# Performance work log

Hardware: AMD Instinct MI355X
Metric: run time of the kernel (lower is better)

The kernel has to match this reference:

```python
import jax, jax.numpy as jnp
import numpy as np

NUM_HEADS = 12
HEAD_DIM = 64
DIM = NUM_HEADS * HEAD_DIM  # 768
WIN = 14
REL = 2 * WIN - 1  # 27


def setup_inputs() -> dict:
    key = jax.random.key(0)
    ks = jax.random.split(key, 7)
    B, N = 256, WIN * WIN
    return {
        "x": jax.random.normal(ks[0], (B, N, DIM), dtype=jnp.float32),
        "qkv_w": jax.random.normal(ks[1], (3 * DIM, DIM), dtype=jnp.float32) * 0.02,
        "qkv_b": jnp.zeros((3 * DIM,), dtype=jnp.float32),
        "rel_pos_h": jax.random.normal(ks[2], (REL, HEAD_DIM), dtype=jnp.float32) * 0.02,
        "rel_pos_w": jax.random.normal(ks[3], (REL, HEAD_DIM), dtype=jnp.float32) * 0.02,
        "proj_w": jax.random.normal(ks[4], (DIM, DIM), dtype=jnp.float32) * 0.02,
        "proj_b": jnp.zeros((DIM,), dtype=jnp.float32),
        "H": WIN,
        "W": WIN,
    }


def _rel_pos_bias(q, rel_pos_h, rel_pos_w, H, W):
    # q: [B, heads, H*W, d] (already scaled). q_shape == k_shape == (H, W), ratios == 1.
    dist_h = jnp.arange(H)[:, None] - jnp.arange(H)[None, :] + (H - 1)  # [H, H]
    dist_w = jnp.arange(W)[:, None] - jnp.arange(W)[None, :] + (W - 1)  # [W, W]
    Rh = rel_pos_h[dist_h]  # [H, H, d]
    Rw = rel_pos_w[dist_w]  # [W, W, d]
    B, nh = q.shape[0], q.shape[1]
    r_q = q.reshape(B, nh, H, W, q.shape[-1])
    rel_h = jnp.einsum("bnhwd,hkd->bnhwk", r_q, Rh)  # [B, nh, H, W, Hk]
    rel_w = jnp.einsum("bnhwd,wkd->bnhwk", r_q, Rw)  # [B, nh, H, W, Wk]
    return rel_h[..., :, None] + rel_w[..., None, :]  # [B, nh, H, W, Hk, Wk]


def reference(x, qkv_w, qkv_b, rel_pos_h, rel_pos_w, proj_w, proj_b, H, W):
    B, N, C = x.shape
    d = C // NUM_HEADS
    scale = d ** -0.5
    qkv = x @ qkv_w.T + qkv_b  # [B, N, 3C]
    qkv = qkv.reshape(B, N, 3, NUM_HEADS, d).transpose(2, 0, 3, 1, 4)
    q, k, v = qkv[0], qkv[1], qkv[2]  # [B, nh, N, d]
    q = q * scale
    attn = jnp.einsum("bhqd,bhkd->bhqk", q, k)  # [B, nh, N, N]
    bias = _rel_pos_bias(q, rel_pos_h, rel_pos_w, H, W)
    attn = (attn.reshape(B, NUM_HEADS, H, W, H, W) + bias).reshape(B, NUM_HEADS, N, N)
    attn = jax.nn.softmax(attn, axis=-1)
    out = jnp.einsum("bhqk,bhkd->bhqd", attn, v)  # [B, nh, N, d]
    out = out.transpose(0, 2, 1, 3).reshape(B, N, C)
    return out @ proj_w.T + proj_b
```

## Files before the change

kernel.cpp:

```cpp
#include <hip/hip_runtime.h>
#include <stdint.h>


typedef __attribute__((ext_vector_type(8))) short bf16x8;
typedef __attribute__((ext_vector_type(4))) float f32x4;
typedef unsigned short u16;
typedef unsigned int u32;

__device__ __forceinline__ u16 f2bf(float f) {
  u32 x = __float_as_uint(f);
  x += 0x7fffu + ((x >> 16) & 1u);
  return (u16)(x >> 16);
}

__device__ __forceinline__ void gload_lds16(const void* g, void* l) {
  __builtin_amdgcn_global_load_lds(
      (__attribute__((address_space(1))) void*)g,
      (__attribute__((address_space(3))) void*)l, 16, 0, 0);
}

__global__ __launch_bounds__(256) void cvt_bf16(const float* __restrict__ src,
                                                u16* __restrict__ dst, int n4) {
  int i = blockIdx.x * 256 + threadIdx.x;
  if (i < n4) {
    float4 f = ((const float4*)src)[i];
    uint2 p;
    p.x = (u32)f2bf(f.x) | ((u32)f2bf(f.y) << 16);
    p.y = (u32)f2bf(f.z) | ((u32)f2bf(f.w) << 16);
    ((uint2*)dst)[i] = p;
  }
}

template <int MODE>
__global__ __launch_bounds__(256) void gemm128(
    const u16* __restrict__ A, const u16* __restrict__ W,
    const float* __restrict__ bias, u16* __restrict__ qb, u16* __restrict__ kb,
    u16* __restrict__ vb, float* __restrict__ outf) {
  __shared__ u16 As[128 * 32];
  __shared__ u16 Bs[128 * 32];
  const int t = threadIdx.x;
  const int m0 = blockIdx.y << 7;
  const int n0 = blockIdx.x << 7;
  const int lane = t & 63, wv = t >> 6;
  const int quad = lane >> 4, l15 = lane & 15;
  const int wm = (wv >> 1) << 6, wn = (wv & 1) << 6;

  f32x4 acc[4][4];
#pragma unroll
  for (int i = 0; i < 4; i++)
#pragma unroll
    for (int j = 0; j < 4; j++) acc[i][j] = (f32x4){0.f, 0.f, 0.f, 0.f};

  const int c0 = t, c1 = t + 256;
  const u16* gA0 = A + (size_t)(m0 + (c0 >> 2)) * 768 + (c0 & 3) * 8;
  const u16* gA1 = A + (size_t)(m0 + (c1 >> 2)) * 768 + (c1 & 3) * 8;
  const u16* gB0 = W + (size_t)(n0 + (c0 >> 2)) * 768 + (c0 & 3) * 8;
  const u16* gB1 = W + (size_t)(n0 + (c1 >> 2)) * 768 + (c1 & 3) * 8;
  u16* lA0 = As + c0 * 8;  u16* lA1 = As + c1 * 8;
  u16* lB0 = Bs + c0 * 8;  u16* lB1 = Bs + c1 * 8;

  const u16* pA = As + (wm + l15) * 32 + quad * 8;
  const u16* pB = Bs + (wn + l15) * 32 + quad * 8;

  for (int k0 = 0; k0 < 768; k0 += 32) {
    __syncthreads();
    gload_lds16(gA0 + k0, lA0);
    gload_lds16(gA1 + k0, lA1);
    gload_lds16(gB0 + k0, lB0);
    gload_lds16(gB1 + k0, lB1);
    __syncthreads();
    bf16x8 af[4], bfr[4];
#pragma unroll
    for (int i = 0; i < 4; i++) af[i] = *(const bf16x8*)(pA + i * 16 * 32);
#pragma unroll
    for (int j = 0; j < 4; j++) bfr[j] = *(const bf16x8*)(pB + j * 16 * 32);
#pragma unroll
    for (int i = 0; i < 4; i++)
#pragma unroll
      for (int j = 0; j < 4; j++)
        acc[i][j] =
            __builtin_amdgcn_mfma_f32_16x16x32_bf16(af[i], bfr[j], acc[i][j], 0, 0, 0);
  }

  if (MODE == 0) {
#pragma unroll
    for (int j = 0; j < 4; j++) {
      int n = n0 + wn + j * 16 + l15;
      int which = n / 768;
      int cc = n - which * 768;
      int head = cc >> 6, dch = cc & 63;
      float bs = bias[n];
      u16* dst = (which == 0) ? qb : ((which == 1) ? kb : vb);
      float sc = (which == 0) ? 0.125f : 1.0f;
#pragma unroll
      for (int i = 0; i < 4; i++) {
#pragma unroll
        for (int r = 0; r < 4; r++) {
          int m = m0 + wm + i * 16 + (quad << 2) + r;
          int bb = m / 196, tok = m - bb * 196;
          float v = (acc[i][j][r] + bs) * sc;
          dst[((size_t)(bb * 12 + head) * 196 + tok) * 64 + dch] = f2bf(v);
        }
      }
    }
  } else {
#pragma unroll
    for (int j = 0; j < 4; j++) {
      int n = n0 + wn + j * 16 + l15;
      float bs = bias[n];
#pragma unroll
      for (int i = 0; i < 4; i++) {
#pragma unroll
        for (int r = 0; r < 4; r++) {
          int m = m0 + wm + i * 16 + (quad << 2) + r;
          outf[(size_t)m * 768 + n] = acc[i][j][r] + bs;
        }
      }
    }
  }
}

__global__ __launch_bounds__(256) void attn_fused(
    const u16* __restrict__ qbuf, const u16* __restrict__ kbuf,
    const u16* __restrict__ vbuf, const float* __restrict__ rel_h,
    const float* __restrict__ rel_w, u16* __restrict__ aout) {
  __shared__ u16 Vt[26 * 512];
  __shared__ u16 PsArr[4 * 26 * 128];

  const int t = threadIdx.x;
  const int bh = blockIdx.x;
  const int b = bh / 12, h = bh - b * 12;
  const int lane = t & 63, wv = t >> 6;
  const int quad = lane >> 4, l15 = lane & 15;
  const size_t base = (size_t)bh * (196 * 64);

  u16* Ps = PsArr + wv * (26 * 128);
  float* Tf = (float*)Ps;

  for (int c = t; c < 196 * 8; c += 256) {
    int row = c >> 3, seg = c & 7;
    uint4 vv = *(const uint4*)(vbuf + base + row * 64 + seg * 8);
    const u16* pv8 = (const u16*)&vv;
    u16* dst = Vt + (row >> 3) * 512 + (row & 7);
#pragma unroll
    for (int e = 0; e < 8; e++) dst[(seg * 8 + e) * 8] = pv8[e];
  }
  for (int i = t; i < 12 * 64; i += 256) {
    int k = 196 + (i >> 6), d = i & 63;
    Vt[(k >> 3) * 512 + d * 8 + (k & 7)] = 0;
  }

  bf16x8 brl[2][2][2];
#pragma unroll
  for (int half = 0; half < 2; half++) {
    const float* relp = half ? rel_w : rel_h;
#pragma unroll
    for (int nt = 0; nt < 2; nt++) {
      int ridx = nt * 16 + l15;
      if (ridx > 26) ridx = 26;
#pragma unroll
      for (int ks = 0; ks < 2; ks++) {
        const float* p = relp + ridx * 64 + ks * 32 + quad * 8;
        float4 f0 = *(const float4*)p;
        float4 f1 = *(const float4*)(p + 4);
        bf16x8 r;
        r[0] = (short)f2bf(f0.x); r[1] = (short)f2bf(f0.y);
        r[2] = (short)f2bf(f0.z); r[3] = (short)f2bf(f0.w);
        r[4] = (short)f2bf(f1.x); r[5] = (short)f2bf(f1.y);
        r[6] = (short)f2bf(f1.z); r[7] = (short)f2bf(f1.w);
        brl[half][nt][ks] = r;
      }
    }
  }
  __syncthreads();

  for (int qt = wv; qt < 13; qt += 4) {
    int qrl = qt * 16 + l15;
    if (qrl > 195) qrl = 195;
    bf16x8 aq0 = *(const bf16x8*)(qbuf + base + qrl * 64 + quad * 8);
    bf16x8 aq1 = *(const bf16x8*)(qbuf + base + qrl * 64 + 32 + quad * 8);

#pragma unroll
    for (int half = 0; half < 2; half++) {
#pragma unroll
      for (int nt = 0; nt < 2; nt++) {
        f32x4 tc = (f32x4){0.f, 0.f, 0.f, 0.f};
        tc = __builtin_amdgcn_mfma_f32_16x16x32_bf16(aq0, brl[half][nt][0], tc, 0, 0, 0);
        tc = __builtin_amdgcn_mfma_f32_16x16x32_bf16(aq1, brl[half][nt][1], tc, 0, 0, 0);
        int col = nt * 16 + l15;
        if (col < 27) {
#pragma unroll
          for (int r = 0; r < 4; r++)
            Tf[half * 448 + (quad * 4 + r) * 28 + col] = tc[r];
        }
      }
    }

    int trow[4], hqv[4], wqv[4];
#pragma unroll
    for (int r = 0; r < 4; r++) {
      int qr = qt * 16 + quad * 4 + r;
      if (qr > 195) qr = 195;
      hqv[r] = qr / 14;
      wqv[r] = qr - hqv[r] * 14;
      trow[r] = (quad * 4 + r) * 28;
    }

    u32 pw2[13][2];
    float sm[4] = {0.f, 0.f, 0.f, 0.f};
#pragma unroll
    for (int kt = 0; kt < 13; kt++) {
      int key = kt * 16 + l15;
      int keyc = (key > 195) ? 195 : key;
      bool valid = (key < 196);
      bf16x8 bk0 = *(const bf16x8*)(kbuf + base + keyc * 64 + quad * 8);
      bf16x8 bk1 = *(const bf16x8*)(kbuf + base + keyc * 64 + 32 + quad * 8);
      f32x4 s = (f32x4){0.f, 0.f, 0.f, 0.f};
      s = __builtin_amdgcn_mfma_f32_16x16x32_bf16(aq0, bk0, s, 0, 0, 0);
      s = __builtin_amdgcn_mfma_f32_16x16x32_bf16(aq1, bk1, s, 0, 0, 0);
      int hk = keyc / 14, wk = keyc - hk * 14;
      float pr[4];
#pragma unroll
      for (int r = 0; r < 4; r++) {
        float v = s[r] + Tf[trow[r] + (hqv[r] - hk + 13)] +
                  Tf[448 + trow[r] + (wqv[r] - wk + 13)];
        float p = valid ? __expf(v) : 0.f;
        pr[r] = p;
        sm[r] += p;
      }
      pw2[kt][0] = (u32)f2bf(pr[0]) | ((u32)f2bf(pr[1]) << 16);
      pw2[kt][1] = (u32)f2bf(pr[2]) | ((u32)f2bf(pr[3]) << 16);
    }

#pragma unroll
    for (int r = 0; r < 4; r++) {
      sm[r] += __shfl_xor(sm[r], 1, 64);
      sm[r] += __shfl_xor(sm[r], 2, 64);
      sm[r] += __shfl_xor(sm[r], 4, 64);
      sm[r] += __shfl_xor(sm[r], 8, 64);
    }
    float inv[4];
#pragma unroll
    for (int r = 0; r < 4; r++) inv[r] = 1.0f / sm[r];

#pragma unroll
    for (int kt = 0; kt < 13; kt++) {
      u16* pp = Ps + (kt * 2 + (l15 >> 3)) * 128 + (l15 & 7);
      pp[(quad * 4 + 0) * 8] = (u16)(pw2[kt][0] & 0xffff);
      pp[(quad * 4 + 1) * 8] = (u16)(pw2[kt][0] >> 16);
      pp[(quad * 4 + 2) * 8] = (u16)(pw2[kt][1] & 0xffff);
      pp[(quad * 4 + 3) * 8] = (u16)(pw2[kt][1] >> 16);
    }

    f32x4 oacc[4];
#pragma unroll
    for (int dt = 0; dt < 4; dt++) oacc[dt] = (f32x4){0.f, 0.f, 0.f, 0.f};
#pragma unroll
    for (int ks = 0; ks < 7; ks++) {
      bool mvalid = (ks < 6) || (quad < 2);
      bf16x8 ap = (bf16x8){0, 0, 0, 0, 0, 0, 0, 0};
      if (mvalid) ap = *(const bf16x8*)(Ps + (ks * 4 + quad) * 128 + l15 * 8);
#pragma unroll
      for (int dt = 0; dt < 4; dt++) {
        bf16x8 bv = (bf16x8){0, 0, 0, 0, 0, 0, 0, 0};
        if (mvalid)
          bv = *(const bf16x8*)(Vt + (ks * 4 + quad) * 512 + (dt * 16 + l15) * 8);
        oacc[dt] = __builtin_amdgcn_mfma_f32_16x16x32_bf16(ap, bv, oacc[dt], 0, 0, 0);
      }
    }

#pragma unroll
    for (int dt = 0; dt < 4; dt++) {
#pragma unroll
      for (int r = 0; r < 4; r++) {
        int qrow = qt * 16 + quad * 4 + r;
        if (qrow < 196) {
          float val = oacc[dt][r] * inv[r];
          aout[((size_t)(b * 196 + qrow) * 12 + h) * 64 + dt * 16 + l15] = f2bf(val);
        }
      }
    }
  }
}

extern "C" void kernel_launch(void* const* d_in, const int* in_sizes, int n_in,
                              void* d_out, int out_size, void* d_ws, size_t ws_size,
                              hipStream_t stream) {
  (void)in_sizes; (void)n_in; (void)out_size; (void)ws_size;
  const float* x      = (const float*)d_in[0];
  const float* qkv_w  = (const float*)d_in[1];
  const float* qkv_b  = (const float*)d_in[2];
  const float* rel_h  = (const float*)d_in[3];
  const float* rel_w  = (const float*)d_in[4];
  const float* proj_w = (const float*)d_in[5];
  const float* proj_b = (const float*)d_in[6];
  float* out = (float*)d_out;

  char* ws = (char*)d_ws;
  u16* xbf  = (u16*)(ws);
  u16* qbuf = (u16*)(ws + 77070336);
  u16* kbuf = (u16*)(ws + 154140672);
  u16* vbuf = (u16*)(ws + 231211008);
  u16* wqb  = (u16*)(ws + 308281344);
  u16* wpb  = (u16*)(ws + 311820288);

  cvt_bf16<<<37632, 256, 0, stream>>>(x, xbf, 38535168 / 4);
  cvt_bf16<<<1728, 256, 0, stream>>>(qkv_w, wqb, 1769472 / 4);
  cvt_bf16<<<576, 256, 0, stream>>>(proj_w, wpb, 589824 / 4);

  gemm128<0><<<dim3(18, 392), 256, 0, stream>>>(xbf, wqb, qkv_b, qbuf, kbuf, vbuf,
                                                nullptr);
  attn_fused<<<3072, 256, 0, stream>>>(qbuf, kbuf, vbuf, rel_h, rel_w, xbf);
  gemm128<1><<<dim3(6, 392), 256, 0, stream>>>(xbf, wpb, proj_b, nullptr, nullptr,
                                               nullptr, out);
}
```

Baseline: 947.3 us.

## Replace 128x128 GEMMs with double-buffered 256x256 tile GEMM with XCD swizzle

Both projection GEMMs now use a 256x256 tile with 512 threads, 64-wide K steps and double-buffered LDS loaded through global_load_lds. The LDS layout is XOR-swizzled to avoid bank conflicts, and the workgroup index is remapped across XCDs for L2 locality. Fragment loads are interleaved with MFMA phases under s_setprio, so the next K tile prefetches while the current one computes. The larger tile cuts global traffic per FLOP, but it uses 128KB of LDS and many accumulator registers, which limits occupancy.

```diff
diff --git a/kernel.cpp b/kernel.cpp
--- a/kernel.cpp
+++ b/kernel.cpp
@@ -31,90 +31,182 @@
   }
 }
 
-template <int MODE>
-__global__ __launch_bounds__(256) void gemm128(
+__device__ __forceinline__ void stage8(const u16* pA, const u16* pB,
+                                       char* dstA, int k0) {
+#pragma unroll
+  for (int i = 0; i < 4; i++)
+    gload_lds16(pA + (size_t)i * 49152 + k0, dstA + i * 8192);
+#pragma unroll
+  for (int i = 0; i < 4; i++)
+    gload_lds16(pB + (size_t)i * 49152 + k0, dstA + 32768 + i * 8192);
+}
+
+template <int MODE, int NT>
+__global__ __launch_bounds__(512, 2) void gemm256(
     const u16* __restrict__ A, const u16* __restrict__ W,
     const float* __restrict__ bias, u16* __restrict__ qb, u16* __restrict__ kb,
     u16* __restrict__ vb, float* __restrict__ outf) {
-  __shared__ u16 As[128 * 32];
-  __shared__ u16 Bs[128 * 32];
+  __shared__ char lds[131072];
+
   const int t = threadIdx.x;
-  const int m0 = blockIdx.y << 7;
-  const int n0 = blockIdx.x << 7;
   const int lane = t & 63, wv = t >> 6;
   const int quad = lane >> 4, l15 = lane & 15;
-  const int wm = (wv >> 1) << 6, wn = (wv & 1) << 6;
-
-  f32x4 acc[4][4];
-#pragma unroll
-  for (int i = 0; i < 4; i++)
+  const int wm = wv >> 2, wn = wv & 3;
+
+  const u32 nwg = gridDim.x;
+  const u32 wg = blockIdx.x;
+  const u32 qd = nwg >> 3, rm = nwg & 7;
+  const u32 xcd = wg & 7, loc = wg >> 3;
+  const u32 swz = (xcd < rm) ? (xcd * (qd + 1) + loc)
+                             : (rm * (qd + 1) + (xcd - rm) * qd + loc);
+  const int mtile = swz / NT;
+  const int ntile = (int)swz - mtile * NT;
+  const int m0 = mtile << 8, n0 = ntile << 8;
+
+  const int srow = t >> 3;
+  const int scol = ((t & 7) ^ (srow & 7)) << 3;
+  const u16* pA = A + (size_t)(m0 + srow) * 768 + scol;
+  const u16* pB = W + (size_t)(n0 + srow) * 768 + scol;
+  char* sdst = lds + t * 16;
+
+  const int swz0 = ((quad) ^ (l15 & 7)) << 4;
+  const int swz1 = ((4 + quad) ^ (l15 & 7)) << 4;
+  const int arow = (wm * 128 + l15) * 128;
+  const int brow = 32768 + (wn * 64 + l15) * 128;
+
+  f32x4 acc[8][4];
+#pragma unroll
+  for (int i = 0; i < 8; i++)
 #pragma unroll
     for (int j = 0; j < 4; j++) acc[i][j] = (f32x4){0.f, 0.f, 0.f, 0.f};
 
-  const int c0 = t, c1 = t + 256;
-  const u16* gA0 = A + (size_t)(m0 + (c0 >> 2)) * 768 + (c0 & 3) * 8;
-  const u16* gA1 = A + (size_t)(m0 + (c1 >> 2)) * 768 + (c1 & 3) * 8;
-  const u16* gB0 = W + (size_t)(n0 + (c0 >> 2)) * 768 + (c0 & 3) * 8;
-  const u16* gB1 = W + (size_t)(n0 + (c1 >> 2)) * 768 + (c1 & 3) * 8;
-  u16* lA0 = As + c0 * 8;  u16* lA1 = As + c1 * 8;
-  u16* lB0 = Bs + c0 * 8;  u16* lB1 = Bs + c1 * 8;
-
-  const u16* pA = As + (wm + l15) * 32 + quad * 8;
-  const u16* pB = Bs + (wn + l15) * 32 + quad * 8;
-
-  for (int k0 = 0; k0 < 768; k0 += 32) {
-    __syncthreads();
-    gload_lds16(gA0 + k0, lA0);
-    gload_lds16(gA1 + k0, lA1);
-    gload_lds16(gB0 + k0, lB0);
-    gload_lds16(gB1 + k0, lB1);
-    __syncthreads();
-    bf16x8 af[4], bfr[4];
-#pragma unroll
-    for (int i = 0; i < 4; i++) af[i] = *(const bf16x8*)(pA + i * 16 * 32);
-#pragma unroll
-    for (int j = 0; j < 4; j++) bfr[j] = *(const bf16x8*)(pB + j * 16 * 32);
-#pragma unroll
-    for (int i = 0; i < 4; i++)
-#pragma unroll
-      for (int j = 0; j < 4; j++)
-        acc[i][j] =
-            __builtin_amdgcn_mfma_f32_16x16x32_bf16(af[i], bfr[j], acc[i][j], 0, 0, 0);
+  stage8(pA, pB, sdst, 0);
+  asm volatile("s_waitcnt vmcnt(0)" ::: "memory");
+  __builtin_amdgcn_s_barrier();
+
+  bf16x8 af[4][2], bfr[4][2];
+  for (int kt = 0; kt < 12; ++kt) {
+    char* bufc = lds + ((kt & 1) << 16);
+    char* nsdst = sdst + (((kt & 1) ^ 1) << 16);
+    const int k0n = (kt + 1) << 6;
+
+#pragma unroll
+    for (int mf = 0; mf < 4; mf++) {
+      af[mf][0] = *(const bf16x8*)(bufc + arow + mf * 2048 + swz0);
+      af[mf][1] = *(const bf16x8*)(bufc + arow + mf * 2048 + swz1);
+    }
+#pragma unroll
+    for (int nf = 0; nf < 2; nf++) {
+      bfr[nf][0] = *(const bf16x8*)(bufc + brow + nf * 2048 + swz0);
+      bfr[nf][1] = *(const bf16x8*)(bufc + brow + nf * 2048 + swz1);
+    }
+    if (kt < 11) stage8(pA, pB, nsdst, k0n);
+    __builtin_amdgcn_s_barrier();
+    asm volatile("s_waitcnt lgkmcnt(0)" ::: "memory");
+    __builtin_amdgcn_s_setprio(1);
+#pragma unroll
+    for (int k = 0; k < 2; k++)
+#pragma unroll
+      for (int mf = 0; mf < 4; mf++)
+#pragma unroll
+        for (int nf = 0; nf < 2; nf++)
+          acc[mf][nf] = __builtin_amdgcn_mfma_f32_16x16x32_bf16(
+              af[mf][k], bfr[nf][k], acc[mf][nf], 0, 0, 0);
+    __builtin_amdgcn_s_setprio(0);
+    __builtin_amdgcn_s_barrier();
+
+#pragma unroll
+    for (int nf = 2; nf < 4; nf++) {
+      bfr[nf][0] = *(const bf16x8*)(bufc + brow + nf * 2048 + swz0);
+      bfr[nf][1] = *(const bf16x8*)(bufc + brow + nf * 2048 + swz1);
+    }
+    __builtin_amdgcn_s_barrier();
+    asm volatile("s_waitcnt lgkmcnt(0)" ::: "memory");
+    __builtin_amdgcn_s_setprio(1);
+#pragma unroll
+    for (int k = 0; k < 2; k++)
+#pragma unroll
+      for (int mf = 0; mf < 4; mf++)
+#pragma unroll
+        for (int nf = 2; nf < 4; nf++)
+          acc[mf][nf] = __builtin_amdgcn_mfma_f32_16x16x32_bf16(
+              af[mf][k], bfr[nf][k], acc[mf][nf], 0, 0, 0);
+    __builtin_amdgcn_s_setprio(0);
+    __builtin_amdgcn_s_barrier();
+
+#pragma unroll
+    for (int mf = 0; mf < 4; mf++) {
+      af[mf][0] = *(const bf16x8*)(bufc + arow + (mf + 4) * 2048 + swz0);
+      af[mf][1] = *(const bf16x8*)(bufc + arow + (mf + 4) * 2048 + swz1);
+    }
+    __builtin_amdgcn_s_barrier();
+    asm volatile("s_waitcnt lgkmcnt(0)" ::: "memory");
+    __builtin_amdgcn_s_setprio(1);
+#pragma unroll
+    for (int k = 0; k < 2; k++)
+#pragma unroll
+      for (int mf = 0; mf < 4; mf++)
+#pragma unroll
+        for (int nf = 0; nf < 2; nf++)
+          acc[mf + 4][nf] = __builtin_amdgcn_mfma_f32_16x16x32_bf16(
+              af[mf][k], bfr[nf][k], acc[mf + 4][nf], 0, 0, 0);
+    __builtin_amdgcn_s_setprio(0);
+    __builtin_amdgcn_s_barrier();
+
+    __builtin_amdgcn_s_setprio(1);
+#pragma unroll
+    for (int k = 0; k < 2; k++)
+#pragma unroll
+      for (int mf = 0; mf < 4; mf++)
+#pragma unroll
+        for (int nf = 2; nf < 4; nf++)
+          acc[mf + 4][nf] = __builtin_amdgcn_mfma_f32_16x16x32_bf16(
+              af[mf][k], bfr[nf][k], acc[mf + 4][nf], 0, 0, 0);
+    __builtin_amdgcn_s_setprio(0);
+    asm volatile("s_waitcnt vmcnt(0)" ::: "memory");
+    __builtin_amdgcn_s_barrier();
   }
 
   if (MODE == 0) {
-#pragma unroll
-    for (int j = 0; j < 4; j++) {
-      int n = n0 + wn + j * 16 + l15;
-      int which = n / 768;
+    const int which = n0 / 768;
+    u16* dst = (which == 0) ? qb : ((which == 1) ? kb : vb);
+    const float sc = (which == 0) ? 0.125f : 1.0f;
+    float bs[4];
+    size_t hb[4];
+#pragma unroll
+    for (int nf = 0; nf < 4; nf++) {
+      int n = n0 + wn * 64 + nf * 16 + l15;
       int cc = n - which * 768;
-      int head = cc >> 6, dch = cc & 63;
-      float bs = bias[n];
-      u16* dst = (which == 0) ? qb : ((which == 1) ? kb : vb);
-      float sc = (which == 0) ? 0.125f : 1.0f;
-#pragma unroll
-      for (int i = 0; i < 4; i++) {
-#pragma unroll
-        for (int r = 0; r < 4; r++) {
-          int m = m0 + wm + i * 16 + (quad << 2) + r;
-          int bb = m / 196, tok = m - bb * 196;
-          float v = (acc[i][j][r] + bs) * sc;
-          dst[((size_t)(bb * 12 + head) * 196 + tok) * 64 + dch] = f2bf(v);
-        }
+      bs[nf] = bias[n];
+      hb[nf] = (size_t)(cc >> 6) * 12544 + (size_t)(cc & 63);
+    }
+#pragma unroll
+    for (int mf = 0; mf < 8; mf++) {
+#pragma unroll
+      for (int r = 0; r < 4; r++) {
+        int m = m0 + wm * 128 + mf * 16 + (quad << 2) + r;
+        int bb = m / 196;
+        int tok = m - bb * 196;
+        size_t rb = (size_t)bb * 150528 + (size_t)tok * 64;
+#pragma unroll
+        for (int nf = 0; nf < 4; nf++)
+          dst[rb + hb[nf]] = f2bf((acc[mf][nf][r] + bs[nf]) * sc);
       }
     }
   } else {
-#pragma unroll
-    for (int j = 0; j < 4; j++) {
-      int n = n0 + wn + j * 16 + l15;
-      float bs = bias[n];
-#pragma unroll
-      for (int i = 0; i < 4; i++) {
-#pragma unroll
-        for (int r = 0; r < 4; r++) {
-          int m = m0 + wm + i * 16 + (quad << 2) + r;
-          outf[(size_t)m * 768 + n] = acc[i][j][r] + bs;
-        }
+    float bs[4];
+#pragma unroll
+    for (int nf = 0; nf < 4; nf++)
+      bs[nf] = bias[n0 + wn * 64 + nf * 16 + l15];
+#pragma unroll
+    for (int mf = 0; mf < 8; mf++) {
+#pragma unroll
+      for (int r = 0; r < 4; r++) {
+        int m = m0 + wm * 128 + mf * 16 + (quad << 2) + r;
+#pragma unroll
+        for (int nf = 0; nf < 4; nf++)
+          outf[(size_t)m * 768 + (n0 + wn * 64 + nf * 16 + l15)] =
+              acc[mf][nf][r] + bs[nf];
       }
     }
   }
@@ -308,9 +400,9 @@
   cvt_bf16<<<1728, 256, 0, stream>>>(qkv_w, wqb, 1769472 / 4);
   cvt_bf16<<<576, 256, 0, stream>>>(proj_w, wpb, 589824 / 4);
 
-  gemm128<0><<<dim3(18, 392), 256, 0, stream>>>(xbf, wqb, qkv_b, qbuf, kbuf, vbuf,
-                                                nullptr);
+  gemm256<0, 9><<<1764, 512, 0, stream>>>(xbf, wqb, qkv_b, qbuf, kbuf, vbuf,
+                                          nullptr);
   attn_fused<<<3072, 256, 0, stream>>>(qbuf, kbuf, vbuf, rel_h, rel_w, xbf);
-  gemm128<1><<<dim3(6, 392), 256, 0, stream>>>(xbf, wpb, proj_b, nullptr, nullptr,
-                                               nullptr, out);
-}
+  gemm256<1, 3><<<588, 512, 0, stream>>>(xbf, wpb, proj_b, nullptr, nullptr,
+                                         nullptr, out);
+}
```

Result: faster. 840.3 us (-11.3%).
